# Optimization experiments

Hardware: AMD Instinct MI355X
Metric: run time of the kernel (lower is better)

Reference implementation:

```python
import jax, jax.numpy as jnp
import numpy as np

GROUP_SIZE = 128
OUT_F, IN_F = 4096, 4096
B, S = 4, 2048


@jax.custom_vjp
def ste_sign(x):
    return jnp.sign(x)

def _ste_fwd(x):
    return jnp.sign(x), None

def _ste_bwd(_, g):
    return (g,)  # straight-through: identity gradient

ste_sign.defvjp(_ste_fwd, _ste_bwd)


def setup_inputs() -> dict:
    key = jax.random.key(0)
    k1, k2, k3 = jax.random.split(key, 3)
    x = jax.random.normal(k1, (B, S, IN_F), dtype=jnp.float32)
    # sign weights are +/-1.0 (zeros mapped to +1, as in the torch init)
    sw = jnp.sign(jax.random.normal(k2, (OUT_F, IN_F), dtype=jnp.float32))
    sign_weights = jnp.where(sw == 0, 1.0, sw)
    # frozen per-group scales (mean |w| per group of 128); positive values
    scales = jax.random.uniform(k3, (OUT_F * IN_F // GROUP_SIZE,), dtype=jnp.float32,
                                minval=0.005, maxval=0.05)
    return {"x": x, "sign_weights": sign_weights, "scales": scales}


def reference(x, sign_weights, scales):
    # binary = sign(sign_weights) with STE (identity grad)
    binary = ste_sign(sign_weights)
    # expand per-group scales: repeat each scale GROUP_SIZE times, view as (out, in)
    scale_mat = jnp.repeat(scales, GROUP_SIZE).reshape(OUT_F, IN_F)
    weight = binary * scale_mat  # [out_f, in_f]
    # F.linear(x, weight) = x @ weight.T
    return jnp.einsum('bsi,oi->bso', x, weight.astype(x.dtype))
```

## Files before the change

kernel.cpp:

```cpp
#include <hip/hip_runtime.h>

#define K_DIM 4096
#define N_DIM 4096
#define M_DIM 8192

typedef __bf16 bf16;
typedef __attribute__((ext_vector_type(8))) __bf16 bf16x8;
typedef __attribute__((ext_vector_type(16))) float f32x16;
typedef __attribute__((ext_vector_type(8))) unsigned short u16x8;

__device__ inline unsigned short f2bf(float f) {
    unsigned u = __builtin_bit_cast(unsigned, f);
    u += 0x7fffu + ((u >> 16) & 1u);
    return (unsigned short)(u >> 16);
}

__global__ __launch_bounds__(256) void prep_kernel(const float* __restrict__ x,
                                                   const float* __restrict__ sw,
                                                   const float* __restrict__ scales,
                                                   unsigned short* __restrict__ oA,
                                                   unsigned short* __restrict__ oW) {
    const int b = blockIdx.x;
    if (b < 16384) {
        const size_t i = (size_t)b * 256 + threadIdx.x;
        const float4* p = (const float4*)x + i * 2;
        float4 a = p[0], c = p[1];
        u16x8 v;
        v[0] = f2bf(a.x); v[1] = f2bf(a.y); v[2] = f2bf(a.z); v[3] = f2bf(a.w);
        v[4] = f2bf(c.x); v[5] = f2bf(c.y); v[6] = f2bf(c.z); v[7] = f2bf(c.w);
        *((u16x8*)oA + i) = v;
    } else {
        const size_t i = (size_t)(b - 16384) * 256 + threadIdx.x;
        const float s = scales[i >> 4];
        const float4* p = (const float4*)sw + i * 2;
        float4 a = p[0], c = p[1];
        u16x8 v;
        v[0] = f2bf(a.x * s); v[1] = f2bf(a.y * s); v[2] = f2bf(a.z * s); v[3] = f2bf(a.w * s);
        v[4] = f2bf(c.x * s); v[5] = f2bf(c.y * s); v[6] = f2bf(c.z * s); v[7] = f2bf(c.w * s);
        *((u16x8*)oW + i) = v;
    }
}

__device__ inline void gll16(const bf16* g, bf16* l) {
    __builtin_amdgcn_global_load_lds(
        (const __attribute__((address_space(1))) void*)g,
        (__attribute__((address_space(3))) void*)l, 16, 0, 0);
}

__global__ __launch_bounds__(256, 2) void gemm_bt_kernel(const bf16* __restrict__ A,
                                                         const bf16* __restrict__ W,
                                                         float* __restrict__ C) {
    __shared__ bf16 As[256 * 64];
    __shared__ bf16 Bs[128 * 64];

    const int t = threadIdx.x;
    const int m0 = blockIdx.y * 256;
    const int n0 = blockIdx.x * 128;
    const int lane = t & 63;
    const int w = t >> 6;
    const int wm = (w >> 1) * 128;
    const int wn = (w & 1) * 64;
    const int ln = lane & 31;
    const int hl = lane >> 5;

    f32x16 acc[4][2] = {};

    const int srow = t >> 3;
    const int scol = (t & 7) ^ (srow & 7);
    const bf16* ga = A + (size_t)(m0 + srow) * K_DIM + scol * 8;
    const bf16* gb = W + (size_t)(n0 + srow) * K_DIM + scol * 8;
    bf16* la = As + t * 8;
    bf16* lb = Bs + t * 8;

    int co[4];
#pragma unroll
    for (int ks = 0; ks < 4; ++ks) co[ks] = ((ks * 2 + hl) ^ (ln & 7)) * 8;
    const bf16* paRow = As + (wm + ln) * 64;
    const bf16* pbRow = Bs + (wn + ln) * 64;

    for (int kb = 0; kb < K_DIM; kb += 64) {
#pragma unroll
        for (int j = 0; j < 8; ++j)
            gll16(ga + kb + (size_t)(32 * j) * K_DIM, la + j * 2048);
#pragma unroll
        for (int j = 0; j < 4; ++j)
            gll16(gb + kb + (size_t)(32 * j) * K_DIM, lb + j * 2048);
        __syncthreads();

#pragma unroll
        for (int ks = 0; ks < 4; ++ks) {
            bf16x8 af[4], bfr[2];
#pragma unroll
            for (int mi = 0; mi < 4; ++mi)
                af[mi] = *(const bf16x8*)(paRow + mi * 2048 + co[ks]);
#pragma unroll
            for (int ni = 0; ni < 2; ++ni)
                bfr[ni] = *(const bf16x8*)(pbRow + ni * 2048 + co[ks]);
#pragma unroll
            for (int mi = 0; mi < 4; ++mi)
#pragma unroll
                for (int ni = 0; ni < 2; ++ni)
                    acc[mi][ni] = __builtin_amdgcn_mfma_f32_32x32x16_bf16(
                        af[mi], bfr[ni], acc[mi][ni], 0, 0, 0);
        }
        __syncthreads();
    }

    float* Cb = C + (size_t)(m0 + wm) * N_DIM + n0 + wn;
#pragma unroll
    for (int mi = 0; mi < 4; ++mi)
#pragma unroll
        for (int ni = 0; ni < 2; ++ni)
#pragma unroll
            for (int r = 0; r < 16; ++r) {
                const int row = mi * 32 + (r & 3) + 8 * (r >> 2) + 4 * hl;
                Cb[(size_t)row * N_DIM + ni * 32 + ln] = acc[mi][ni][r];
            }
}

extern "C" void kernel_launch(void* const* d_in, const int* in_sizes, int n_in,
                              void* d_out, int out_size, void* d_ws, size_t ws_size,
                              hipStream_t stream) {
    const float* x      = (const float*)d_in[0];
    const float* sw     = (const float*)d_in[1];
    const float* scales = (const float*)d_in[2];
    float* out = (float*)d_out;

    bf16* Abf = (bf16*)d_ws;
    bf16* Wbf = (bf16*)((char*)d_ws + (size_t)M_DIM * K_DIM * 2);

    prep_kernel<<<24576, 256, 0, stream>>>(x, sw, scales,
                                           (unsigned short*)Abf, (unsigned short*)Wbf);

    dim3 grid(N_DIM / 128, M_DIM / 256);
    gemm_bt_kernel<<<grid, 256, 0, stream>>>(Abf, Wbf, out);
}
```

Before: 517.0 us.

## Rewrite GEMM as 256x256 tile, 8-wave, double-buffered LDS pipeline with XCD swizzle

Grows the GEMM tile to 256x256 with 512 threads and double-buffered dynamic LDS. Global-to-LDS loads for later k-steps are interleaved with MFMA quarter-blocks under explicit waitcnt, barriers and setprio. Block IDs are remapped across XCDs to improve L2 reuse, and the prep kernel now processes 16 floats per thread using nontemporal loads. The aim is to hide memory latency and cut global traffic per FLOP, at the cost of fragile hand-written scheduling and higher LDS use, which may reduce occupancy.

Result: no change. 508.4 us (-1.7%).

```diff
diff --git a/kernel.cpp b/kernel.cpp
--- a/kernel.cpp
+++ b/kernel.cpp
@@ -7,6 +7,7 @@
 typedef __bf16 bf16;
 typedef __attribute__((ext_vector_type(8))) __bf16 bf16x8;
 typedef __attribute__((ext_vector_type(16))) float f32x16;
+typedef __attribute__((ext_vector_type(4))) float fv4;
 typedef __attribute__((ext_vector_type(8))) unsigned short u16x8;
 
 __device__ inline unsigned short f2bf(float f) {
@@ -21,23 +22,35 @@
                                                    unsigned short* __restrict__ oA,
                                                    unsigned short* __restrict__ oW) {
     const int b = blockIdx.x;
-    if (b < 16384) {
-        const size_t i = (size_t)b * 256 + threadIdx.x;
-        const float4* p = (const float4*)x + i * 2;
-        float4 a = p[0], c = p[1];
-        u16x8 v;
-        v[0] = f2bf(a.x); v[1] = f2bf(a.y); v[2] = f2bf(a.z); v[3] = f2bf(a.w);
-        v[4] = f2bf(c.x); v[5] = f2bf(c.y); v[6] = f2bf(c.z); v[7] = f2bf(c.w);
-        *((u16x8*)oA + i) = v;
+    if (b < 8192) {
+        const size_t T = (size_t)b * 256 + threadIdx.x;
+        const fv4* p = (const fv4*)x + T * 4;
+        const fv4 a = __builtin_nontemporal_load(p);
+        const fv4 c = __builtin_nontemporal_load(p + 1);
+        const fv4 d = __builtin_nontemporal_load(p + 2);
+        const fv4 e = __builtin_nontemporal_load(p + 3);
+        u16x8 v0, v1;
+        v0[0] = f2bf(a[0]); v0[1] = f2bf(a[1]); v0[2] = f2bf(a[2]); v0[3] = f2bf(a[3]);
+        v0[4] = f2bf(c[0]); v0[5] = f2bf(c[1]); v0[6] = f2bf(c[2]); v0[7] = f2bf(c[3]);
+        v1[0] = f2bf(d[0]); v1[1] = f2bf(d[1]); v1[2] = f2bf(d[2]); v1[3] = f2bf(d[3]);
+        v1[4] = f2bf(e[0]); v1[5] = f2bf(e[1]); v1[6] = f2bf(e[2]); v1[7] = f2bf(e[3]);
+        u16x8* o = (u16x8*)oA + T * 2;
+        o[0] = v0; o[1] = v1;
     } else {
-        const size_t i = (size_t)(b - 16384) * 256 + threadIdx.x;
-        const float s = scales[i >> 4];
-        const float4* p = (const float4*)sw + i * 2;
-        float4 a = p[0], c = p[1];
-        u16x8 v;
-        v[0] = f2bf(a.x * s); v[1] = f2bf(a.y * s); v[2] = f2bf(a.z * s); v[3] = f2bf(a.w * s);
-        v[4] = f2bf(c.x * s); v[5] = f2bf(c.y * s); v[6] = f2bf(c.z * s); v[7] = f2bf(c.w * s);
-        *((u16x8*)oW + i) = v;
+        const size_t T = (size_t)(b - 8192) * 256 + threadIdx.x;
+        const float s = scales[T >> 3];
+        const fv4* p = (const fv4*)sw + T * 4;
+        const fv4 a = __builtin_nontemporal_load(p);
+        const fv4 c = __builtin_nontemporal_load(p + 1);
+        const fv4 d = __builtin_nontemporal_load(p + 2);
+        const fv4 e = __builtin_nontemporal_load(p + 3);
+        u16x8 v0, v1;
+        v0[0] = f2bf(a[0] * s); v0[1] = f2bf(a[1] * s); v0[2] = f2bf(a[2] * s); v0[3] = f2bf(a[3] * s);
+        v0[4] = f2bf(c[0] * s); v0[5] = f2bf(c[1] * s); v0[6] = f2bf(c[2] * s); v0[7] = f2bf(c[3] * s);
+        v1[0] = f2bf(d[0] * s); v1[1] = f2bf(d[1] * s); v1[2] = f2bf(d[2] * s); v1[3] = f2bf(d[3] * s);
+        v1[4] = f2bf(e[0] * s); v1[5] = f2bf(e[1] * s); v1[6] = f2bf(e[2] * s); v1[7] = f2bf(e[3] * s);
+        u16x8* o = (u16x8*)oW + T * 2;
+        o[0] = v0; o[1] = v1;
     }
 }
 
@@ -47,66 +60,147 @@
         (__attribute__((address_space(3))) void*)l, 16, 0, 0);
 }
 
-__global__ __launch_bounds__(256, 2) void gemm_bt_kernel(const bf16* __restrict__ A,
+extern __shared__ __align__(16) bf16 lds[];
+
+#define BAR __builtin_amdgcn_s_barrier()
+#define SB0 __builtin_amdgcn_sched_barrier(0)
+#define STAGE(gbase, kofs, ldst)                                       \
+    do {                                                               \
+        gll16((gbase) + (kofs), (ldst));                               \
+        gll16((gbase) + (size_t)128 * K_DIM + (kofs), (ldst) + 4096);  \
+    } while (0)
+
+__device__ __forceinline__ void mm8(f32x16 (&acc)[4][2], int mib,
+                                    bf16x8 (&af)[2][2], bf16x8 (&bv)[2][2]) {
+#pragma unroll
+    for (int ks = 0; ks < 2; ++ks)
+#pragma unroll
+        for (int mi = 0; mi < 2; ++mi)
+#pragma unroll
+            for (int ni = 0; ni < 2; ++ni)
+                acc[mib + mi][ni] = __builtin_amdgcn_mfma_f32_32x32x16_bf16(
+                    af[mi][ks], bv[ni][ks], acc[mib + mi][ni], 0, 0, 0);
+}
+
+template <int BUF, bool I1, bool I2, int VM>
+__device__ __forceinline__ void kgroup(f32x16 (&acc)[4][2], const bf16* fA,
+                                       const bf16* fB, const int* co, const bf16* gA,
+                                       const bf16* gB, bf16* lA, bf16* lB, int ko1,
+                                       int ko2) {
+    const bf16* rA = fA + BUF * 32768;
+    const bf16* rB = fB + BUF * 32768;
+    bf16x8 a01[2][2], a23[2][2], bv[2][2], a01h[2][2], a23h[2][2], bvh[2][2];
+
+#pragma unroll
+    for (int mi = 0; mi < 2; ++mi)
+#pragma unroll
+        for (int ks = 0; ks < 2; ++ks) a01[mi][ks] = *(const bf16x8*)(rA + mi * 1024 + co[ks]);
+#pragma unroll
+    for (int ni = 0; ni < 2; ++ni)
+#pragma unroll
+        for (int ks = 0; ks < 2; ++ks) bv[ni][ks] = *(const bf16x8*)(rB + ni * 1024 + co[ks]);
+    SB0;
+#pragma unroll
+    for (int mi = 0; mi < 2; ++mi)
+#pragma unroll
+        for (int ks = 0; ks < 2; ++ks)
+            a23[mi][ks] = *(const bf16x8*)(rA + (2 + mi) * 1024 + co[ks]);
+    if (I1) STAGE(gB, ko1, lB + (1 - BUF) * 32768 + 8192);
+    BAR;
+    asm volatile("s_waitcnt lgkmcnt(4)" ::: "memory"); SB0;
+    __builtin_amdgcn_s_setprio(1); mm8(acc, 0, a01, bv); __builtin_amdgcn_s_setprio(0);
+    BAR;
+
+#pragma unroll
+    for (int mi = 0; mi < 2; ++mi)
+#pragma unroll
+        for (int ks = 0; ks < 2; ++ks)
+            a01h[mi][ks] = *(const bf16x8*)(rA + 8192 + mi * 1024 + co[ks]);
+#pragma unroll
+    for (int ni = 0; ni < 2; ++ni)
+#pragma unroll
+        for (int ks = 0; ks < 2; ++ks)
+            bvh[ni][ks] = *(const bf16x8*)(rB + 8192 + ni * 1024 + co[ks]);
+#pragma unroll
+    for (int mi = 0; mi < 2; ++mi)
+#pragma unroll
+        for (int ks = 0; ks < 2; ++ks)
+            a23h[mi][ks] = *(const bf16x8*)(rA + 8192 + (2 + mi) * 1024 + co[ks]);
+    if (I2) STAGE(gB, ko2, lB + BUF * 32768);
+    BAR;
+    asm volatile("s_waitcnt lgkmcnt(12)" ::: "memory"); SB0;
+    __builtin_amdgcn_s_setprio(1); mm8(acc, 2, a23, bv); __builtin_amdgcn_s_setprio(0);
+    BAR;
+
+    if (I2) STAGE(gA, ko2, lA + BUF * 32768);
+    BAR;
+    asm volatile("s_waitcnt lgkmcnt(0)" ::: "memory"); SB0;
+    __builtin_amdgcn_s_setprio(1); mm8(acc, 0, a01h, bvh); __builtin_amdgcn_s_setprio(0);
+    BAR;
+
+    if (I2) STAGE(gA, ko2 + 32, lA + BUF * 32768 + 8192);
+    BAR;
+    asm volatile("s_waitcnt lgkmcnt(0)" ::: "memory"); SB0;
+    __builtin_amdgcn_s_setprio(1); mm8(acc, 2, a23h, bvh); __builtin_amdgcn_s_setprio(0);
+    if (VM == 6) asm volatile("s_waitcnt vmcnt(6)" ::: "memory");
+    if (VM == 0) asm volatile("s_waitcnt vmcnt(0)" ::: "memory");
+    BAR;
+}
+
+__global__ __launch_bounds__(512, 2) void gemm_bt_kernel(const bf16* __restrict__ A,
                                                          const bf16* __restrict__ W,
                                                          float* __restrict__ C) {
-    __shared__ bf16 As[256 * 64];
-    __shared__ bf16 Bs[128 * 64];
+    const int raw = blockIdx.x;
+    const int swz = (raw & 7) * 64 + (raw >> 3);
+    const int m0 = (swz >> 4) * 256;
+    const int n0 = (swz & 15) * 256;
 
     const int t = threadIdx.x;
-    const int m0 = blockIdx.y * 256;
-    const int n0 = blockIdx.x * 128;
     const int lane = t & 63;
     const int w = t >> 6;
-    const int wm = (w >> 1) * 128;
-    const int wn = (w & 1) * 64;
-    const int ln = lane & 31;
+    const int wm = w >> 2;
+    const int wn = w & 3;
+    const int l31 = lane & 31;
     const int hl = lane >> 5;
 
+    const int srow = t >> 2;
+    const int slb = ((t & 3) ^ ((t >> 3) & 3)) * 8;
+    const bf16* gA = A + (size_t)(m0 + srow) * K_DIM + slb;
+    const bf16* gB = W + (size_t)(n0 + srow) * K_DIM + slb;
+    bf16* lA = lds + t * 8;
+    bf16* lB = lds + 16384 + t * 8;
+
+    int co[2];
+#pragma unroll
+    for (int ks = 0; ks < 2; ++ks) co[ks] = ((ks * 2 + hl) ^ ((l31 >> 1) & 3)) * 8;
+    const bf16* fA = lds + (wm * 128 + l31) * 32;
+    const bf16* fB = lds + 16384 + (wn * 64 + l31) * 32;
+
     f32x16 acc[4][2] = {};
 
-    const int srow = t >> 3;
-    const int scol = (t & 7) ^ (srow & 7);
-    const bf16* ga = A + (size_t)(m0 + srow) * K_DIM + scol * 8;
-    const bf16* gb = W + (size_t)(n0 + srow) * K_DIM + scol * 8;
-    bf16* la = As + t * 8;
-    bf16* lb = Bs + t * 8;
-
-    int co[4];
-#pragma unroll
-    for (int ks = 0; ks < 4; ++ks) co[ks] = ((ks * 2 + hl) ^ (ln & 7)) * 8;
-    const bf16* paRow = As + (wm + ln) * 64;
-    const bf16* pbRow = Bs + (wn + ln) * 64;
-
-    for (int kb = 0; kb < K_DIM; kb += 64) {
-#pragma unroll
-        for (int j = 0; j < 8; ++j)
-            gll16(ga + kb + (size_t)(32 * j) * K_DIM, la + j * 2048);
-#pragma unroll
-        for (int j = 0; j < 4; ++j)
-            gll16(gb + kb + (size_t)(32 * j) * K_DIM, lb + j * 2048);
-        __syncthreads();
-
-#pragma unroll
-        for (int ks = 0; ks < 4; ++ks) {
-            bf16x8 af[4], bfr[2];
-#pragma unroll
-            for (int mi = 0; mi < 4; ++mi)
-                af[mi] = *(const bf16x8*)(paRow + mi * 2048 + co[ks]);
-#pragma unroll
-            for (int ni = 0; ni < 2; ++ni)
-                bfr[ni] = *(const bf16x8*)(pbRow + ni * 2048 + co[ks]);
-#pragma unroll
-            for (int mi = 0; mi < 4; ++mi)
-#pragma unroll
-                for (int ni = 0; ni < 2; ++ni)
-                    acc[mi][ni] = __builtin_amdgcn_mfma_f32_32x32x16_bf16(
-                        af[mi], bfr[ni], acc[mi][ni], 0, 0, 0);
-        }
-        __syncthreads();
+    STAGE(gA, 0, lA);
+    STAGE(gB, 0, lB);
+    STAGE(gA, 32, lA + 8192);
+    STAGE(gB, 32, lB + 8192);
+    STAGE(gB, 64, lB + 32768);
+    STAGE(gA, 64, lA + 32768);
+    STAGE(gA, 96, lA + 32768 + 8192);
+    asm volatile("s_waitcnt vmcnt(6)" ::: "memory");
+    BAR;
+
+    int ko1 = 96;
+    int ko2 = 128;
+#pragma unroll 1
+    for (int gg = 0; gg < 31; ++gg) {
+        kgroup<0, true, true, 6>(acc, fA, fB, co, gA, gB, lA, lB, ko1, ko2);
+        ko1 += 64; ko2 += 64;
+        kgroup<1, true, true, 6>(acc, fA, fB, co, gA, gB, lA, lB, ko1, ko2);
+        ko1 += 64; ko2 += 64;
     }
-
-    float* Cb = C + (size_t)(m0 + wm) * N_DIM + n0 + wn;
+    kgroup<0, true, false, 0>(acc, fA, fB, co, gA, gB, lA, lB, ko1, ko2);
+    kgroup<1, false, false, -1>(acc, fA, fB, co, gA, gB, lA, lB, 0, 0);
+
+    float* Cb = C + (size_t)(m0 + wm * 128) * N_DIM + n0 + wn * 64;
 #pragma unroll
     for (int mi = 0; mi < 4; ++mi)
 #pragma unroll
@@ -114,24 +208,30 @@
 #pragma unroll
             for (int r = 0; r < 16; ++r) {
                 const int row = mi * 32 + (r & 3) + 8 * (r >> 2) + 4 * hl;
-                Cb[(size_t)row * N_DIM + ni * 32 + ln] = acc[mi][ni][r];
+                Cb[(size_t)row * N_DIM + ni * 32 + l31] = acc[mi][ni][r];
             }
 }
 
 extern "C" void kernel_launch(void* const* d_in, const int* in_sizes, int n_in,
                               void* d_out, int out_size, void* d_ws, size_t ws_size,
                               hipStream_t stream) {
-    const float* x      = (const float*)d_in[0];
-    const float* sw     = (const float*)d_in[1];
+    const float* x = (const float*)d_in[0];
+    const float* sw = (const float*)d_in[1];
     const float* scales = (const float*)d_in[2];
     float* out = (float*)d_out;
 
     bf16* Abf = (bf16*)d_ws;
     bf16* Wbf = (bf16*)((char*)d_ws + (size_t)M_DIM * K_DIM * 2);
 
-    prep_kernel<<<24576, 256, 0, stream>>>(x, sw, scales,
+    static int lds_set = 0;
+    if (!lds_set) {
+        (void)hipFuncSetAttribute((const void*)gemm_bt_kernel,
+                                  hipFuncAttributeMaxDynamicSharedMemorySize, 131072);
+        lds_set = 1;
+    }
+
+    prep_kernel<<<12288, 256, 0, stream>>>(x, sw, scales,
                                            (unsigned short*)Abf, (unsigned short*)Wbf);
 
-    dim3 grid(N_DIM / 128, M_DIM / 256);
-    gemm_bt_kernel<<<grid, 256, 0, stream>>>(Abf, Wbf, out);
-}
+    gemm_bt_kernel<<<dim3(N_DIM / 256 * (M_DIM / 256)), 512, 131072, stream>>>(Abf, Wbf, out);
+}
```
